# Optimization experiments

Measured on AMD Instinct MI355X. Metric: run time of the kernel, lower is better.

The kernel has to match this reference:

```python
import jax, jax.numpy as jnp
import numpy as np

N, D = 4096, 256  # num_nodes, hidden_dim (num_layers = 1)

def setup_inputs() -> dict:
    key = jax.random.key(0)
    ks = jax.random.split(key, 7)
    s = 0.05  # small init scale so the LSTM gates stay in a sane range
    return {
        "h":    jax.random.normal(ks[0], (N, D), dtype=jnp.float32),
        "W_ih": jax.random.normal(ks[1], (4 * D, 2 * D), dtype=jnp.float32) * s,
        "W_hh": jax.random.normal(ks[2], (4 * D, D), dtype=jnp.float32) * s,
        "b_ih": jax.random.normal(ks[3], (4 * D,), dtype=jnp.float32) * s,
        "b_hh": jax.random.normal(ks[4], (4 * D,), dtype=jnp.float32) * s,
        "W_a":  jax.random.normal(ks[5], (D, D), dtype=jnp.float32) * s,
        "b_a":  jax.random.normal(ks[6], (D,), dtype=jnp.float32) * s,
    }

def reference(h, W_ih, W_hh, b_ih, b_hh, W_a, b_a):
    num_nodes, d = h.shape

    def step(carry, _):
        hs, cs, q_star = carry  # hs, cs: (1, D); q_star: (1, 2D)
        # single-layer torch LSTM cell, gate order i, f, g, o
        gates = q_star @ W_ih.T + b_ih + hs @ W_hh.T + b_hh  # (1, 4D)
        i, f, g, o = jnp.split(gates, 4, axis=-1)
        c_new = jax.nn.sigmoid(f) * cs + jax.nn.sigmoid(i) * jnp.tanh(g)
        q = jax.nn.sigmoid(o) * jnp.tanh(c_new)              # (1, D)
        # attention read over all nodes
        e = h @ (q @ W_a.T + b_a)[0]                          # (N,)
        a = jax.nn.softmax(e, axis=0)                         # (N,)
        r = (a @ h)[None, :]                                  # (1, D)
        q_star_new = jnp.concatenate([q, r], axis=-1)         # (1, 2D)
        return (q, c_new, q_star_new), None

    init = (jnp.zeros((1, d), h.dtype), jnp.zeros((1, d), h.dtype),
            jnp.zeros((1, 2 * d), h.dtype))
    (hs, cs, q_star), _ = jax.lax.scan(step, init, None, length=num_nodes)
    return q_star
```

## Files before the change

kernel.cpp:

```cpp
#include <hip/hip_runtime.h>
#include <stdint.h>

#define NN 4096
#define DD 256
#define NWG 64
#define TT 256
#define ROWS 64
#define GR 16
#define NSTEPS 4096
#define GUARD (1u << 20)

typedef float f32x4 __attribute__((ext_vector_type(4)));

#define OFF_HDR      0u
#define OFF_QS       4096u
#define OFF_SCAL     12288u
#define OFF_PR       12352u
#define OFF_EB       77888u
#define OFF_BPACK    94272u
#define OFF_WPACK    98368u
#define OFF_HPB      2195520u
#define OFF_HP2      4292672u

#define S_HPL    0u
#define S_HP     32768u
#define S_WL     65536u
#define S_QRL    98816u
#define S_PRL    100864u
#define S_RACC   104960u
#define S_EL     106048u
#define S_PL     107072u
#define S_GL     107328u
#define S_CLS    107392u
#define S_RED4   107408u
#define S_SL     107424u
#define S_EBL    107440u
#define S_QL4    107696u
#define SMEM_BYTES 107712

__device__ __forceinline__ float bf2f(unsigned short u) {
  return __uint_as_float(((unsigned)u) << 16);
}
__device__ __forceinline__ unsigned short f2bf(float f) {
  unsigned x = __float_as_uint(f);
  unsigned r = x + 0x7fffu + ((x >> 16) & 1u);
  return (unsigned short)(r >> 16);
}

__device__ __forceinline__ f32x4 ld_v4(const void* p) {
  f32x4 v;
  asm volatile("global_load_dwordx4 %0, %1, off sc0 sc1\n\ts_waitcnt vmcnt(0)"
               : "=v"(v) : "v"(p) : "memory");
  return v;
}
__device__ __forceinline__ f32x4 ld_v4_async(const void* p) {
  f32x4 v;
  asm volatile("global_load_dwordx4 %0, %1, off sc0 sc1" : "=v"(v) : "v"(p) : "memory");
  return v;
}
__device__ __forceinline__ void st_v4(void* p, f32x4 v) {
  asm volatile("global_store_dwordx4 %0, %1, off sc0 sc1" :: "v"(p), "v"(v) : "memory");
}
__device__ __forceinline__ void vmdrain() {
  asm volatile("s_waitcnt vmcnt(0)" ::: "memory");
}
__device__ __forceinline__ void npause() { __builtin_amdgcn_s_sleep(1); }

__global__ void k0_init(char* ws) {
  int t = threadIdx.x;
  unsigned* u = (unsigned*)ws;
  float* f = (float*)ws;
  for (int i = t; i < 64; i += TT) {
    u[(OFF_HDR >> 2) + i * 16] = 0u;
    f[(OFF_HDR >> 2) + i * 16 + 1] = 1.0f / NWG;
  }
  for (int i = t; i < 64; i += TT) {
    u[(OFF_QS >> 2) + i * 32] = 0u;
    u[(OFF_QS >> 2) + i * 32 + 16] = 0u;
  }
  if (t == 0) { u[OFF_SCAL / 4] = 0u; u[OFF_SCAL / 4 + 1] = 0u; }
  for (int i = t; i < 64 * 256; i += TT) f[(OFF_PR >> 2) + i] = 0.f;
}

__global__ __launch_bounds__(256) void k1_hp(const float* __restrict__ h,
                                             const float* __restrict__ W_a,
                                             const float* __restrict__ b_a,
                                             char* ws) {
  __shared__ float hL1[16][256];
  __shared__ float scr[16][256];
  __shared__ float redN[4][16];
  __shared__ float redE[4][16];
  const int t = threadIdx.x, b = blockIdx.x;
  const int i0 = b * 16;
  for (int i = t; i < 16 * 256; i += 256) hL1[i >> 8][i & 255] = h[i0 * 256 + i];
  __syncthreads();
  float acc[16];
#pragma unroll
  for (int ii = 0; ii < 16; ++ii) acc[ii] = 0.f;
  for (int j = 0; j < 256; ++j) {
    float wa = W_a[j * 256 + t];
#pragma unroll
    for (int ii = 0; ii < 16; ++ii) acc[ii] += hL1[ii][j] * wa;
  }
#pragma unroll
  for (int ii = 0; ii < 16; ++ii) scr[ii][t] = acc[ii];
  const int lane = t & 63, wv = t >> 6;
  const float ba = b_a[t];
  for (int ii = 0; ii < 16; ++ii) {
    float a2 = acc[ii] * acc[ii];
    float eb = hL1[ii][t] * ba;
    for (int m = 32; m; m >>= 1) { a2 += __shfl_xor(a2, m); eb += __shfl_xor(eb, m); }
    if (lane == 0) { redN[wv][ii] = a2; redE[wv][ii] = eb; }
  }
  __syncthreads();
  unsigned* scal = (unsigned*)(ws + OFF_SCAL);
  float* ebg = (float*)(ws + OFF_EB);
  if (t < 16) {
    float n2 = redN[0][t] + redN[1][t] + redN[2][t] + redN[3][t];
    float ebv = redE[0][t] + redE[1][t] + redE[2][t] + redE[3][t];
    ebg[i0 + t] = ebv;
    atomicMax(scal + 0, __float_as_uint(sqrtf(n2)));
    atomicMax(scal + 1, __float_as_uint(fabsf(ebv)));
  }
  uint2* hpB = (uint2*)(ws + OFF_HPB);
  const int wq = b >> 2, sub = b & 3;
  for (int idx = t; idx < 16 * 64; idx += 256) {
    int ii = idx >> 6, k4 = idx & 63;
    unsigned short u0 = f2bf(scr[ii][4 * k4 + 0]);
    unsigned short u1 = f2bf(scr[ii][4 * k4 + 1]);
    unsigned short u2 = f2bf(scr[ii][4 * k4 + 2]);
    unsigned short u3 = f2bf(scr[ii][4 * k4 + 3]);
    uint2 pv;
    pv.x = (unsigned)u0 | ((unsigned)u1 << 16);
    pv.y = (unsigned)u2 | ((unsigned)u3 << 16);
    int rl = sub * 16 + ii;
    hpB[wq * 4096 + k4 * 64 + rl] = pv;
  }
}

__global__ void k2_pack(const float* __restrict__ h, const float* __restrict__ W_ih,
                        const float* __restrict__ W_hh, const float* __restrict__ b_ih,
                        const float* __restrict__ b_hh, char* ws) {
  unsigned* hp2 = (unsigned*)(ws + OFF_HP2);
  float* wpack = (float*)(ws + OFF_WPACK);
  float* bpack = (float*)(ws + OFF_BPACK);
  int idx0 = blockIdx.x * blockDim.x + threadIdx.x;
  int stride = gridDim.x * blockDim.x;
  for (int i = idx0; i < NN * DD / 2; i += stride) {
    int col = i & 255;
    int r2 = (i >> 8) & 31;
    int w = i >> 13;
    int row0 = (w * 64 + 2 * r2) * 256 + col;
    hp2[i] = (unsigned)f2bf(h[row0]) | ((unsigned)f2bf(h[row0 + 256]) << 16);
  }
  for (int i = idx0; i < 1024 * 512; i += stride) {
    int row = i >> 9, c = i & 511;
    int g = row >> 8, d = row & 255;
    int wq = d >> 2, dl = d & 3;
    float v = W_ih[row * 512 + c];
    if (c < 256) v += W_hh[row * 256 + c];
    wpack[(wq * GR + g * 4 + dl) * 512 + c] = v;
  }
  for (int i = idx0; i < 1024; i += stride) {
    int g = i >> 8, d = i & 255, wq = d >> 2, dl = d & 3;
    bpack[wq * GR + g * 4 + dl] = b_ih[i] + b_hh[i];
  }
}

__global__ __launch_bounds__(TT, 1) void s2s_main(char* __restrict__ ws,
                                                  float* __restrict__ out) {
  extern __shared__ char smem[];
  uint2* HpL = (uint2*)(smem + S_HPL);
  unsigned* hP = (unsigned*)(smem + S_HP);
  float* wL = (float*)(smem + S_WL);
  float* qrL = (float*)(smem + S_QRL);
  float* prL = (float*)(smem + S_PRL);
  float* rAcc = (float*)(smem + S_RACC);
  float* eL = (float*)(smem + S_EL);
  float* pL = (float*)(smem + S_PL);
  float* gL = (float*)(smem + S_GL);
  float* cLs = (float*)(smem + S_CLS);
  float* red4 = (float*)(smem + S_RED4);
  float* sL = (float*)(smem + S_SL);
  float* ebL = (float*)(smem + S_EBL);
  float* qL4 = (float*)(smem + S_QL4);

  const int w = blockIdx.x, tid = threadIdx.x;
  char* hdrBase = ws + OFF_HDR;
  char* qsBase = ws + OFF_QS;
  const unsigned* scal = (const unsigned*)(ws + OFF_SCAL);
  float* pr = (float*)(ws + OFF_PR);
  const float* ebg = (const float*)(ws + OFF_EB);
  const float* bpack = (const float*)(ws + OFF_BPACK);
  const float* wpack = (const float*)(ws + OFF_WPACK);
  const uint2* hpB = (const uint2*)(ws + OFF_HPB) + (size_t)w * 4096;
  const unsigned* hp2 = (const unsigned*)(ws + OFF_HP2) + (size_t)w * 8192;

  for (int i = tid; i < 4096; i += TT) HpL[i] = hpB[i];
  for (int i = tid; i < 8192; i += TT) hP[i] = hp2[i];
  for (int i = tid; i < 8192; i += TT) {
    int r = i >> 9, c = i & 511;
    wL[r * 520 + c] = wpack[(size_t)w * 8192 + i];
  }
  if (tid < 64) ebL[tid] = ebg[w * 64 + tid];
  if (tid < 4) cLs[tid] = 0.f;
  qrL[tid] = 0.f;
  qrL[256 + tid] = 0.f;
  const float maxHpN = __uint_as_float(scal[0]);
  const float ebB = __uint_as_float(scal[1]);
  __syncthreads();

  const int gr_lr = tid >> 4, gr_li = tid & 15;
  const float* wrow = wL + gr_lr * 520;
  const float brow = bpack[w * GR + gr_lr];
  const int wv4 = tid >> 6, l = tid & 63;
  float psW = 0.f;

  for (int t = 0; t < NSTEPS; ++t) {
    float acc = 0.f;
#pragma unroll
    for (int j = 0; j < 4; ++j) {
      int c0 = gr_li * 4 + j * 64;
      const float4 wv = *(const float4*)(wrow + c0);
      const float4 qv = *(const float4*)(qrL + c0);
      acc += wv.x * qv.x + wv.y * qv.y + wv.z * qv.z + wv.w * qv.w;
    }
    if (tid < 64) {
      const char* hp = hdrBase + tid * 64;
      float psv;
      unsigned guard = 0;
      for (;;) {
        f32x4 hv = ld_v4(hp);
        if (__float_as_uint(hv.x) >= (unsigned)t || ++guard > GUARD) { psv = hv.y; break; }
        npause();
      }
      float s = psv;
#pragma unroll
      for (int m = 32; m; m >>= 1) s += __shfl_xor(s, m);
      if (tid == 0) sL[0] = fmaxf(s, 1e-35f);
    }
    __syncthreads();
    {
      f32x4 tv[16];
#pragma unroll
      for (int i = 0; i < 16; ++i) {
        int v = (wv4 * 16 + i + w) & 63;
        tv[i] = ld_v4_async(pr + v * 256 + (l << 2));
      }
      vmdrain();
      __builtin_amdgcn_sched_barrier(0);
      float rx = 0.f, ry = 0.f, rz = 0.f, rw = 0.f;
#pragma unroll
      for (int i = 0; i < 16; ++i) { rx += tv[i].x; ry += tv[i].y; rz += tv[i].z; rw += tv[i].w; }
      float* d = prL + wv4 * 256 + (l << 2);
      d[0] = rx; d[1] = ry; d[2] = rz; d[3] = rw;
    }
    __syncthreads();
    {
      float rsum = prL[tid] + prL[256 + tid] + prL[512 + tid] + prL[768 + tid];
      qrL[256 + tid] = rsum / sL[0];
    }
    __syncthreads();
#pragma unroll
    for (int j = 4; j < 8; ++j) {
      int c0 = gr_li * 4 + j * 64;
      const float4 wv = *(const float4*)(wrow + c0);
      const float4 qv = *(const float4*)(qrL + c0);
      acc += wv.x * qv.x + wv.y * qv.y + wv.z * qv.z + wv.w * qv.w;
    }
    acc += __shfl_xor(acc, 8);
    acc += __shfl_xor(acc, 4);
    acc += __shfl_xor(acc, 2);
    acc += __shfl_xor(acc, 1);
    if (gr_li == 0) gL[gr_lr] = acc + brow;
    __syncthreads();
    if (tid < 4) {
      float gi = gL[tid], gf = gL[4 + tid], gg = gL[8 + tid], go = gL[12 + tid];
      float co = cLs[tid];
      float si = 1.f / (1.f + __expf(-gi));
      float sf = 1.f / (1.f + __expf(-gf));
      float so = 1.f / (1.f + __expf(-go));
      float cn = sf * co + si * tanhf(gg);
      cLs[tid] = cn;
      qL4[tid] = so * tanhf(cn);
    }
    if (tid < 2) {
      float4 q4 = *(const float4*)qL4;
      f32x4 line;
      line.x = __uint_as_float((unsigned)(t + 1));
      if (tid == 0) { line.y = q4.x; line.z = q4.y; line.w = q4.z; }
      else          { line.y = q4.w; line.z = 0.f;  line.w = 0.f; }
      st_v4(qsBase + w * 128 + tid * 64, line);
    }

    float nr = 0.f;
    if (l < 32) {
      const int w2 = (wv4 << 4) + (l >> 1);
      const char* qp = qsBase + w2 * 128 + (l & 1) * 64;
      const unsigned need = (unsigned)(t + 1);
      f32x4 qv;
      unsigned guard = 0;
      for (;;) {
        qv = ld_v4(qp);
        if (__float_as_uint(qv.x) >= need || ++guard > GUARD) break;
        npause();
      }
      if ((l & 1) == 0) {
        qrL[4 * w2] = qv.y; qrL[4 * w2 + 1] = qv.z; qrL[4 * w2 + 2] = qv.w;
        nr = qv.y * qv.y + qv.z * qv.z + qv.w * qv.w;
      } else {
        qrL[4 * w2 + 3] = qv.y;
        nr = qv.y * qv.y;
      }
    }
#pragma unroll
    for (int m = 1; m < 64; m <<= 1) nr += __shfl_xor(nr, m);
    if (l == 0) red4[wv4] = nr;
    f32x4 qk[16];
#pragma unroll
    for (int j = 0; j < 16; ++j)
      qk[j] = *(const f32x4*)(qrL + (wv4 << 6) + (j << 2));
    float eacc = 0.f;
#pragma unroll
    for (int j = 0; j < 16; ++j) {
      const uint2 hp = HpL[(((wv4 << 4) + j) << 6) + l];
      eacc += bf2f((unsigned short)(hp.x)) * qk[j].x +
              bf2f((unsigned short)(hp.x >> 16)) * qk[j].y +
              bf2f((unsigned short)(hp.y)) * qk[j].z +
              bf2f((unsigned short)(hp.y >> 16)) * qk[j].w;
    }
    eL[(wv4 << 6) + l] = eacc;
    __syncthreads();
    if (tid < 64) {
      const float qnorm = sqrtf(red4[0] + red4[1] + red4[2] + red4[3]);
      const float Mhat = 0.5f * maxHpN * qnorm + ebB;
      float e = eL[tid] + eL[64 + tid] + eL[128 + tid] + eL[192 + tid] + ebL[tid];
      float p = __expf(fminf(e - Mhat, 60.f));
      pL[tid] = p;
      float sv = p;
#pragma unroll
      for (int m = 32; m; m >>= 1) sv += __shfl_xor(sv, m);
      if (tid == 0) psW = sv;
    }
    __syncthreads();
    float r2 = 0.f;
#pragma unroll
    for (int r2i = 0; r2i < 32; ++r2i) {
      const unsigned hv = hP[(r2i << 8) + tid];
      r2 += pL[2 * r2i] * bf2f((unsigned short)hv) +
            pL[2 * r2i + 1] * bf2f((unsigned short)(hv >> 16));
    }
    rAcc[tid] = r2;
    __syncthreads();
    if (tid < 64) {
      f32x4 pv;
      pv.x = rAcc[4 * tid]; pv.y = rAcc[4 * tid + 1];
      pv.z = rAcc[4 * tid + 2]; pv.w = rAcc[4 * tid + 3];
      st_v4(pr + (w << 8) + (tid << 2), pv);
      vmdrain();
    }
    __syncthreads();
    if (tid == 0) {
      f32x4 hv4;
      hv4.x = __uint_as_float((unsigned)(t + 1));
      hv4.y = psW; hv4.z = 0.f; hv4.w = 0.f;
      st_v4(hdrBase + w * 64, hv4);
    }
  }

  if (w == 0) {
    if (tid < 64) {
      const char* hp = hdrBase + tid * 64;
      float psv;
      unsigned guard = 0;
      for (;;) {
        f32x4 hv = ld_v4(hp);
        if (__float_as_uint(hv.x) >= (unsigned)NSTEPS || ++guard > GUARD) { psv = hv.y; break; }
        npause();
      }
      float s = psv;
#pragma unroll
      for (int m = 32; m; m >>= 1) s += __shfl_xor(s, m);
      if (tid == 0) sL[0] = fmaxf(s, 1e-35f);
    }
    __syncthreads();
    {
      f32x4 tv[16];
#pragma unroll
      for (int i = 0; i < 16; ++i) {
        int v = (wv4 * 16 + i) & 63;
        tv[i] = ld_v4_async(pr + v * 256 + (l << 2));
      }
      vmdrain();
      __builtin_amdgcn_sched_barrier(0);
      float rx = 0.f, ry = 0.f, rz = 0.f, rw = 0.f;
#pragma unroll
      for (int i = 0; i < 16; ++i) { rx += tv[i].x; ry += tv[i].y; rz += tv[i].z; rw += tv[i].w; }
      float* d = prL + wv4 * 256 + (l << 2);
      d[0] = rx; d[1] = ry; d[2] = rz; d[3] = rw;
    }
    __syncthreads();
    float rsum = prL[tid] + prL[256 + tid] + prL[512 + tid] + prL[768 + tid];
    out[tid] = qrL[tid];
    out[256 + tid] = rsum / sL[0];
  }
}

extern "C" void kernel_launch(void* const* d_in, const int* in_sizes, int n_in,
                              void* d_out, int out_size, void* d_ws, size_t ws_size,
                              hipStream_t stream) {
  const float* h = (const float*)d_in[0];
  const float* W_ih = (const float*)d_in[1];
  const float* W_hh = (const float*)d_in[2];
  const float* b_ih = (const float*)d_in[3];
  const float* b_hh = (const float*)d_in[4];
  const float* W_a = (const float*)d_in[5];
  const float* b_a = (const float*)d_in[6];
  char* ws = (char*)d_ws;
  float* out = (float*)d_out;

  (void)hipFuncSetAttribute(reinterpret_cast<const void*>(s2s_main),
                            hipFuncAttributeMaxDynamicSharedMemorySize, SMEM_BYTES);

  k0_init<<<1, TT, 0, stream>>>(ws);
  k1_hp<<<256, 256, 0, stream>>>(h, W_a, b_a, ws);
  k2_pack<<<1024, 256, 0, stream>>>(h, W_ih, W_hh, b_ih, b_hh, ws);
  s2s_main<<<NWG, TT, SMEM_BYTES, stream>>>(ws, out);
}
```

Measured before the change: 25.19 ms.

## Pack step headers densely, poll them in every wave, and hoist next-step gate dot

Per-workgroup step headers are packed into 8-byte slots instead of 64-byte lines. Every wave now polls all 64 headers and reduces the softmax denominator in registers, which removes an LDS broadcast and a barrier. The first half of the next step's gate dot product (over q) is computed before the end-of-step barrier, overlapping it with the drain of the partial-result stores. The trade-off is more redundant polling traffic, and packed headers now share cache lines, so cross-workgroup writes contend on the same lines.

Result: slower. 30.06 ms (+19.3%).

```diff
diff --git a/kernel.cpp b/kernel.cpp
--- a/kernel.cpp
+++ b/kernel.cpp
@@ -11,6 +11,7 @@
 #define GUARD (1u << 20)
 
 typedef float f32x4 __attribute__((ext_vector_type(4)));
+typedef float f32x2 __attribute__((ext_vector_type(2)));
 
 #define OFF_HDR      0u
 #define OFF_QS       4096u
@@ -58,8 +59,17 @@
   asm volatile("global_load_dwordx4 %0, %1, off sc0 sc1" : "=v"(v) : "v"(p) : "memory");
   return v;
 }
+__device__ __forceinline__ f32x2 ld_v2(const void* p) {
+  f32x2 v;
+  asm volatile("global_load_dwordx2 %0, %1, off sc0 sc1\n\ts_waitcnt vmcnt(0)"
+               : "=v"(v) : "v"(p) : "memory");
+  return v;
+}
 __device__ __forceinline__ void st_v4(void* p, f32x4 v) {
   asm volatile("global_store_dwordx4 %0, %1, off sc0 sc1" :: "v"(p), "v"(v) : "memory");
+}
+__device__ __forceinline__ void st_v2(void* p, f32x2 v) {
+  asm volatile("global_store_dwordx2 %0, %1, off sc0 sc1" :: "v"(p), "v"(v) : "memory");
 }
 __device__ __forceinline__ void vmdrain() {
   asm volatile("s_waitcnt vmcnt(0)" ::: "memory");
@@ -71,8 +81,8 @@
   unsigned* u = (unsigned*)ws;
   float* f = (float*)ws;
   for (int i = t; i < 64; i += TT) {
-    u[(OFF_HDR >> 2) + i * 16] = 0u;
-    f[(OFF_HDR >> 2) + i * 16 + 1] = 1.0f / NWG;
+    u[(OFF_HDR >> 2) + i * 2] = 0u;
+    f[(OFF_HDR >> 2) + i * 2 + 1] = 1.0f / NWG;
   }
   for (int i = t; i < 64; i += TT) {
     u[(OFF_QS >> 2) + i * 32] = 0u;
@@ -181,7 +191,6 @@
   float* gL = (float*)(smem + S_GL);
   float* cLs = (float*)(smem + S_CLS);
   float* red4 = (float*)(smem + S_RED4);
-  float* sL = (float*)(smem + S_SL);
   float* ebL = (float*)(smem + S_EBL);
   float* qL4 = (float*)(smem + S_QL4);
 
@@ -215,31 +224,23 @@
   const float brow = bpack[w * GR + gr_lr];
   const int wv4 = tid >> 6, l = tid & 63;
   float psW = 0.f;
+  float acc = 0.f;
 
   for (int t = 0; t < NSTEPS; ++t) {
-    float acc = 0.f;
-#pragma unroll
-    for (int j = 0; j < 4; ++j) {
-      int c0 = gr_li * 4 + j * 64;
-      const float4 wv = *(const float4*)(wrow + c0);
-      const float4 qv = *(const float4*)(qrL + c0);
-      acc += wv.x * qv.x + wv.y * qv.y + wv.z * qv.z + wv.w * qv.w;
-    }
-    if (tid < 64) {
-      const char* hp = hdrBase + tid * 64;
-      float psv;
+    float psTot;
+    {
+      const char* hp = hdrBase + l * 8;
+      f32x2 hv = ld_v2(hp);
       unsigned guard = 0;
-      for (;;) {
-        f32x4 hv = ld_v4(hp);
-        if (__float_as_uint(hv.x) >= (unsigned)t || ++guard > GUARD) { psv = hv.y; break; }
+      while (__float_as_uint(hv.x) < (unsigned)t && ++guard <= GUARD) {
         npause();
-      }
-      float s = psv;
+        hv = ld_v2(hp);
+      }
+      float s = hv.y;
 #pragma unroll
       for (int m = 32; m; m >>= 1) s += __shfl_xor(s, m);
-      if (tid == 0) sL[0] = fmaxf(s, 1e-35f);
-    }
-    __syncthreads();
+      psTot = fmaxf(s, 1e-35f);
+    }
     {
       f32x4 tv[16];
 #pragma unroll
@@ -258,7 +259,7 @@
     __syncthreads();
     {
       float rsum = prL[tid] + prL[256 + tid] + prL[512 + tid] + prL[768 + tid];
-      qrL[256 + tid] = rsum / sL[0];
+      qrL[256 + tid] = rsum / psTot;
     }
     __syncthreads();
 #pragma unroll
@@ -298,12 +299,11 @@
       const int w2 = (wv4 << 4) + (l >> 1);
       const char* qp = qsBase + w2 * 128 + (l & 1) * 64;
       const unsigned need = (unsigned)(t + 1);
-      f32x4 qv;
+      f32x4 qv = ld_v4(qp);
       unsigned guard = 0;
-      for (;;) {
+      while (__float_as_uint(qv.x) < need && ++guard <= GUARD) {
+        npause();
         qv = ld_v4(qp);
-        if (__float_as_uint(qv.x) >= need || ++guard > GUARD) break;
-        npause();
       }
       if ((l & 1) == 0) {
         qrL[4 * w2] = qv.y; qrL[4 * w2 + 1] = qv.z; qrL[4 * w2 + 2] = qv.w;
@@ -357,33 +357,43 @@
       pv.x = rAcc[4 * tid]; pv.y = rAcc[4 * tid + 1];
       pv.z = rAcc[4 * tid + 2]; pv.w = rAcc[4 * tid + 3];
       st_v4(pr + (w << 8) + (tid << 2), pv);
-      vmdrain();
-    }
-    __syncthreads();
-    if (tid == 0) {
-      f32x4 hv4;
-      hv4.x = __uint_as_float((unsigned)(t + 1));
-      hv4.y = psW; hv4.z = 0.f; hv4.w = 0.f;
-      st_v4(hdrBase + w * 64, hv4);
+    }
+    {
+      float accN = 0.f;
+#pragma unroll
+      for (int j = 0; j < 4; ++j) {
+        int c0 = gr_li * 4 + j * 64;
+        const float4 wv = *(const float4*)(wrow + c0);
+        const float4 qv = *(const float4*)(qrL + c0);
+        accN += wv.x * qv.x + wv.y * qv.y + wv.z * qv.z + wv.w * qv.w;
+      }
+      if (tid < 64) vmdrain();
+      __syncthreads();
+      if (tid == 0) {
+        f32x2 hv2;
+        hv2.x = __uint_as_float((unsigned)(t + 1));
+        hv2.y = psW;
+        st_v2(hdrBase + w * 8, hv2);
+      }
+      acc = accN;
     }
   }
 
   if (w == 0) {
-    if (tid < 64) {
-      const char* hp = hdrBase + tid * 64;
-      float psv;
+    float psTot;
+    {
+      const char* hp = hdrBase + l * 8;
+      f32x2 hv = ld_v2(hp);
       unsigned guard = 0;
-      for (;;) {
-        f32x4 hv = ld_v4(hp);
-        if (__float_as_uint(hv.x) >= (unsigned)NSTEPS || ++guard > GUARD) { psv = hv.y; break; }
+      while (__float_as_uint(hv.x) < (unsigned)NSTEPS && ++guard <= GUARD) {
         npause();
-      }
-      float s = psv;
+        hv = ld_v2(hp);
+      }
+      float s = hv.y;
 #pragma unroll
       for (int m = 32; m; m >>= 1) s += __shfl_xor(s, m);
-      if (tid == 0) sL[0] = fmaxf(s, 1e-35f);
-    }
-    __syncthreads();
+      psTot = fmaxf(s, 1e-35f);
+    }
     {
       f32x4 tv[16];
 #pragma unroll
@@ -402,7 +412,7 @@
     __syncthreads();
     float rsum = prL[tid] + prL[256 + tid] + prL[512 + tid] + prL[768 + tid];
     out[tid] = qrL[tid];
-    out[256 + tid] = rsum / sL[0];
+    out[256 + tid] = rsum / psTot;
   }
 }
 
```
